# Performance work log

Measured on AMD Instinct MI355X. Metric: run time of the kernel, lower is better.

## Reference

```python
import jax, jax.numpy as jnp
import numpy as np

B, T, D = 4, 1024, 1024
H = 16
DH = D // H  # 64
NEG = jnp.float32(-2.0**32 + 1)


def _sinusoid_table(T, D):
    pos = np.arange(T)[:, None]
    i = np.arange(D)[None, :]
    angle = pos / np.power(10000.0, 2.0 * (i // 2) / D)
    tab = np.zeros((T, D))
    tab[:, 0::2] = np.sin(angle[:, 0::2])
    tab[:, 1::2] = np.cos(angle[:, 1::2])
    return jnp.asarray(tab, dtype=jnp.float32)


def setup_inputs() -> dict:
    key = jax.random.key(0)
    ks = jax.random.split(key, 10)
    inp = {
        "queries": jax.random.normal(ks[0], (B, T, D), dtype=jnp.float32),
        "keys": jax.random.normal(ks[1], (B, T, D), dtype=jnp.float32),
        "query_lens": jax.random.randint(ks[2], (B, 1), 1, T + 1),
        "key_lens": jax.random.randint(ks[3], (B, 1), 1, T + 1),
        # learned params
        "pe_q": _sinusoid_table(T, D),
        "pe_k": _sinusoid_table(T, D),
        "W_Query": jax.random.truncated_normal(ks[4], -2.0, 2.0, (D, D), dtype=jnp.float32) * 0.05,
        "W_key": jax.random.truncated_normal(ks[5], -2.0, 2.0, (D, D), dtype=jnp.float32) * 0.05,
        "W_Value": jax.random.truncated_normal(ks[6], -2.0, 2.0, (D, D), dtype=jnp.float32) * 0.05,
        "fw1": jax.random.normal(ks[7], (D, 4 * D), dtype=jnp.float32) * (1.0 / np.sqrt(D)),
        "fw2": jax.random.normal(ks[8], (4 * D, D), dtype=jnp.float32) * (1.0 / np.sqrt(4 * D)),
    }
    return inp


def _forward(queries, keys, pe_q, pe_k, W_Query, W_key, W_Value, fw1, fw2,
             query_lens, key_lens):
    scale = jnp.float32(np.sqrt(D))
    # positional encoding (scale=True). NOTE: source bug preserved —
    # keys tensor is overwritten by key_pe applied to the PE'd queries.
    q_in = queries + pe_q[None] * scale          # [B,T,D]
    k_in = q_in + pe_k[None] * scale             # [B,T,D]

    Q = q_in @ W_Query                           # [B,T,D]
    K = k_in @ W_key                             # [B,T,D]
    V = K @ W_Value                              # NOTE: V projected from projected keys (source quirk)

    def heads(x):  # [B,T,D] -> [H,B,T,DH]
        return x.reshape(B, T, H, DH).transpose(2, 0, 1, 3)

    Qh, Kh, Vh = heads(Q), heads(K), heads(V)
    scores = jnp.einsum("hbqd,hbkd->hbqk", Qh, Kh) / jnp.float32(np.sqrt(DH))

    t = jnp.arange(T)
    kmask = (t[None, :] < key_lens).astype(jnp.float32)    # [B,T]
    qmask = (t[None, :] < query_lens).astype(jnp.float32)  # [B,T]

    scores = jnp.where(kmask[None, :, None, :] == 1.0, scores, NEG)
    # blinding: set diagonal to large negative
    eye = jnp.eye(T, dtype=bool)
    scores = jnp.where(eye[None, None], NEG, scores)

    scores = scores - scores.max(axis=-1, keepdims=True)
    probs = jax.nn.softmax(scores, axis=-1)
    probs = probs * qmask[None, :, :, None]

    out = jnp.einsum("hbqk,hbkd->hbqd", probs, Vh)         # [H,B,T,DH]
    result = out.transpose(1, 2, 0, 3).reshape(B, T, D)
    result = result + q_in                                  # residual uses PE'd queries

    ff = jnp.maximum(result @ fw1, 0.0) @ fw2
    result = result + ff
    return result.mean(axis=1, keepdims=True)               # [B,1,D]


def reference(queries, keys, query_lens, key_lens, pe_q, pe_k,
              W_Query, W_key, W_Value, fw1, fw2):
    return _forward(queries, keys, pe_q, pe_k, W_Query, W_key, W_Value,
                    fw1, fw2, query_lens, key_lens)
```

## Files before the change

kernel.cpp:

```cpp
#include <hip/hip_runtime.h>

#define T_ 1024
#define D_ 1024
#define B_ 4
#define H_ 16
#define DH_ 64
#define M_ (B_*T_)
#define NEG_ (-4294967295.0f)

typedef __attribute__((ext_vector_type(8))) _Float16 f16x8;
typedef __attribute__((ext_vector_type(4))) float f32x4;

__device__ __forceinline__ unsigned short f2h(float f) {
    _Float16 h = (_Float16)f; unsigned short u; __builtin_memcpy(&u, &h, 2); return u;
}
__device__ __forceinline__ float h2f(unsigned short u) {
    _Float16 h; __builtin_memcpy(&h, &u, 2); return (float)h;
}

typedef const unsigned int __attribute__((address_space(1)))* gas_p;
typedef unsigned int __attribute__((address_space(3)))* las_p;
__device__ __forceinline__ void gl_lds16(const void* g, void* l) {
    __builtin_amdgcn_global_load_lds((gas_p)g, (las_p)l, 16, 0, 0);
}

__global__ __launch_bounds__(256) void conv_all(const float* __restrict__ q,
                                                const float* __restrict__ peq,
                                                const float* __restrict__ pek,
                                                const float* __restrict__ Wq,
                                                const float* __restrict__ Wk,
                                                const float* __restrict__ Wv,
                                                const float* __restrict__ fw1,
                                                const int* __restrict__ klv,
                                                unsigned short* __restrict__ A2,
                                                unsigned short* __restrict__ B2,
                                                unsigned short* __restrict__ WvT,
                                                unsigned short* __restrict__ fw1T)
{
    int blk = blockIdx.x;
    if (blk < 8192) {
        int i = blk * 256 + threadIdx.x;
        int m = i >> 8, c4 = (i & 255) << 2;
        int mq = m & 4095;
        if (m >= 4096) {
            int row = m - 4096;
            int kl = klv[row >> 10];
            if (kl > 1 && (row & 1023) >= kl) return;
        }
        float4 qv = *(const float4*)(q + (size_t)mq * D_ + c4);
        float4 p  = *(const float4*)(peq + (size_t)(m & (T_-1)) * D_ + c4);
        ushort4 h;
        if (m < 4096) {
            h.x = f2h(qv.x + 32.f*p.x); h.y = f2h(qv.y + 32.f*p.y);
            h.z = f2h(qv.z + 32.f*p.z); h.w = f2h(qv.w + 32.f*p.w);
        } else {
            float4 pk = *(const float4*)(pek + (size_t)(m & (T_-1)) * D_ + c4);
            h.x = f2h(qv.x + 32.f*(p.x + pk.x)); h.y = f2h(qv.y + 32.f*(p.y + pk.y));
            h.z = f2h(qv.z + 32.f*(p.z + pk.z)); h.w = f2h(qv.w + 32.f*(p.w + pk.w));
        }
        *(ushort4*)(A2 + (size_t)m * 1024 + c4) = h;
        return;
    }
    __shared__ float t[32][33];
    int r = threadIdx.x >> 5, c = threadIdx.x & 31;
    if (blk < 10240) {
        int l = blk - 8192;
        int z = l >> 10, k0 = ((l >> 5) & 31) * 32, n0 = (l & 31) * 32;
        const float* W = z ? Wk : Wq;
        #pragma unroll
        for (int rr = 0; rr < 4; ++rr)
            t[r + 8*rr][c] = W[(size_t)(k0 + r + 8*rr) * 1024 + n0 + c];
        __syncthreads();
        #pragma unroll
        for (int rr = 0; rr < 4; ++rr)
            B2[(size_t)(z * 1024 + n0 + r + 8*rr) * 1024 + k0 + c] = f2h(t[c][r + 8*rr]);
    } else if (blk < 11264) {
        int l = blk - 10240;
        int k0 = (l >> 5) * 32, n0 = (l & 31) * 32;
        #pragma unroll
        for (int rr = 0; rr < 4; ++rr)
            t[r + 8*rr][c] = Wv[(size_t)(k0 + r + 8*rr) * 1024 + n0 + c];
        __syncthreads();
        #pragma unroll
        for (int rr = 0; rr < 4; ++rr)
            WvT[(size_t)(n0 + r + 8*rr) * 1024 + k0 + c] = f2h(t[c][r + 8*rr]);
    } else {
        int l = blk - 11264;
        int k0 = (l >> 7) * 32, n0 = (l & 127) * 32;
        #pragma unroll
        for (int rr = 0; rr < 4; ++rr)
            t[r + 8*rr][c] = fw1[(size_t)(k0 + r + 8*rr) * 4096 + n0 + c];
        __syncthreads();
        #pragma unroll
        for (int rr = 0; rr < 4; ++rr)
            fw1T[(size_t)(n0 + r + 8*rr) * 1024 + k0 + c] = f2h(t[c][r + 8*rr]);
    }
}

template<int BM>
__global__ __launch_bounds__(256) void gemm_mfma(
    const unsigned short* __restrict__ A, int lda,
    const unsigned short* __restrict__ B, int ldb, int K,
    unsigned short* __restrict__ outh, unsigned short* __restrict__ outh2,
    int N, int flags,
    const int* __restrict__ qlv, const int* __restrict__ klv)
{
    constexpr int WN = (BM == 128) ? 2 : 4;
    constexpr int FN = 8 / WN;
    constexpr int NA = BM / 32;
    __shared__ __align__(16) unsigned short As[2][BM * 64];
    __shared__ __align__(16) unsigned short Bs[2][128 * 64];
    const int tid = threadIdx.x;
    const int m0 = blockIdx.y * BM, n0 = blockIdx.x << 7;
    if (flags & 32) {
        if (m0 < 4096) {
            if (n0 >= 1024) return;
            if ((m0 & 1023) >= qlv[m0 >> 10]) return;
        } else {
            if (n0 < 1024) return;
            int kl = klv[(m0 - 4096) >> 10];
            if (kl > 1 && (m0 & 1023) >= kl) return;
        }
    }
    if (flags & 256) {
        int bb = m0 >> 10, kl = klv[bb];
        if (kl > 1 && (m0 & 1023) >= kl) return;
    }
    const int lane = tid & 63, wave = tid >> 6;
    const int wm = (wave / WN) * 64;
    const int wn = (wave % WN) * (128 / WN);
    const int rl = lane & 15, kg = lane >> 4;
    const int rl7 = lane & 7;

    int ca[NA]; const unsigned short* gA[NA];
    #pragma unroll
    for (int i = 0; i < NA; ++i) {
        int c = i * 256 + tid;
        int row = c >> 3, k8 = (c & 7) ^ (row & 7);
        ca[i] = c * 8;
        gA[i] = A + (size_t)(m0 + row) * lda + k8 * 8;
    }
    int cb[4]; const unsigned short* gB[4];
    #pragma unroll
    for (int i = 0; i < 4; ++i) {
        int c = i * 256 + tid;
        int row = c >> 3, k8 = (c & 7) ^ (row & 7);
        cb[i] = c * 8;
        gB[i] = B + (size_t)(n0 + row) * ldb + k8 * 8;
    }

    int aoff[2][4], boff[2][FN];
    #pragma unroll
    for (int tt = 0; tt < 2; ++tt) {
        #pragma unroll
        for (int f = 0; f < 4; ++f)
            aoff[tt][f] = (wm + (f << 4) + rl) * 64 + (((tt * 4 + kg) ^ rl7) << 3);
        #pragma unroll
        for (int f = 0; f < FN; ++f)
            boff[tt][f] = (wn + (f << 4) + rl) * 64 + (((tt * 4 + kg) ^ rl7) << 3);
    }

    f32x4 acc[4][FN];
    #pragma unroll
    for (int i = 0; i < 4; ++i)
        #pragma unroll
        for (int j = 0; j < FN; ++j) {
            acc[i][j][0] = 0.f; acc[i][j][1] = 0.f;
            acc[i][j][2] = 0.f; acc[i][j][3] = 0.f;
        }

    const int NT = K >> 6;
    #pragma unroll
    for (int i = 0; i < 4; ++i)  gl_lds16(gB[i], &Bs[0][cb[i]]);
    #pragma unroll
    for (int i = 0; i < NA; ++i) gl_lds16(gA[i], &As[0][ca[i]]);
    #pragma unroll
    for (int i = 0; i < 4; ++i)  gl_lds16(gB[i] + 64, &Bs[1][cb[i]]);
    #pragma unroll
    for (int i = 0; i < NA; ++i) gl_lds16(gA[i] + 64, &As[1][ca[i]]);

    for (int t = 0; t < NT; ++t) {
        const int cur = t & 1;
        if (t + 1 < NT) {
            if constexpr (BM == 128) asm volatile("s_waitcnt vmcnt(8)" ::: "memory");
            else                     asm volatile("s_waitcnt vmcnt(6)" ::: "memory");
        } else {
            asm volatile("s_waitcnt vmcnt(0)" ::: "memory");
        }
        __builtin_amdgcn_s_barrier();
        __builtin_amdgcn_sched_barrier(0);
        f16x8 av[2][4], bv[2][FN];
        #pragma unroll
        for (int tt = 0; tt < 2; ++tt) {
            #pragma unroll
            for (int f = 0; f < 4; ++f)
                av[tt][f] = *(const f16x8*)&As[cur][aoff[tt][f]];
            #pragma unroll
            for (int f = 0; f < FN; ++f)
                bv[tt][f] = *(const f16x8*)&Bs[cur][boff[tt][f]];
        }
        asm volatile("s_waitcnt lgkmcnt(0)" ::: "memory");
        __builtin_amdgcn_sched_barrier(0);
        __builtin_amdgcn_s_barrier();
        __builtin_amdgcn_sched_barrier(0);
        if (t + 2 < NT) {
            const int ko = (t + 2) << 6;
            #pragma unroll
            for (int i = 0; i < 4; ++i)  gl_lds16(gB[i] + ko, &Bs[cur][cb[i]]);
            #pragma unroll
            for (int i = 0; i < NA; ++i) gl_lds16(gA[i] + ko, &As[cur][ca[i]]);
        }
        #pragma unroll
        for (int fm = 0; fm < 4; ++fm)
            #pragma unroll
            for (int fn = 0; fn < FN; ++fn) {
                acc[fm][fn] = __builtin_amdgcn_mfma_f32_16x16x32_f16(av[0][fm], bv[0][fn], acc[fm][fn], 0, 0, 0);
                acc[fm][fn] = __builtin_amdgcn_mfma_f32_16x16x32_f16(av[1][fm], bv[1][fn], acc[fm][fn], 0, 0, 0);
            }
    }

    #pragma unroll
    for (int fm = 0; fm < 4; ++fm) {
        int row = m0 + wm + (fm << 4) + (kg << 2);
        #pragma unroll
        for (int fn = 0; fn < FN; ++fn) {
            int col = n0 + wn + (fn << 4) + rl;
            if (flags & 64) {
                ushort4 u;
                u.x = f2h(acc[fm][fn][0]); u.y = f2h(acc[fm][fn][1]);
                u.z = f2h(acc[fm][fn][2]); u.w = f2h(acc[fm][fn][3]);
                size_t a = ((size_t)((row >> 10) * 16 + (col >> 6)) * 64 + (col & 63)) * 1024 + (row & 1023);
                *(ushort4*)(outh + a) = u;
                continue;
            }
            #pragma unroll
            for (int r = 0; r < 4; ++r) {
                float x = acc[fm][fn][r];
                int rr = row + r;
                if (flags & 32) {
                    if (rr < 4096) outh[(size_t)rr * 1024 + col] = f2h(x);
                    else           outh2[(size_t)(rr - 4096) * 1024 + (col - 1024)] = f2h(x);
                } else if (flags & 16) {
                    outh[(size_t)rr * N + col] = f2h(x);
                }
            }
        }
    }
}

__global__ __launch_bounds__(512, 2) void ffn1_8p(
    const unsigned short* __restrict__ A,
    const unsigned short* __restrict__ B,
    float* __restrict__ hpart)
{
    __shared__ __align__(16) unsigned short As[2][16384];
    __shared__ __align__(16) unsigned short Bs[2][16384];
    __shared__ float hp[8][64];
    const int tid = threadIdx.x;
    const int m0 = blockIdx.y << 8, n0 = blockIdx.x << 8;
    const int lane = tid & 63, wave = tid >> 6;
    const int wm = wave >> 2, wn = wave & 3;
    const int rl = lane & 15, kg = lane >> 4, rl7 = lane & 7;

    const int row0 = tid >> 3;
    const int k8c = (tid & 7) ^ (row0 & 7);
    const int cs0 = tid * 8;
    const int gofs = row0 * 1024 + k8c * 8;
    const unsigned short* Ap = A + (size_t)m0 * 1024 + gofs;
    const unsigned short* Bp = B + (size_t)n0 * 1024 + gofs;

    const int base_a = ((wm * 128 + rl) * 8 + (kg ^ rl7)) * 8;
    const int base_b = (((wn >> 1) * 128 + (wn & 1) * 64 + rl) * 8 + (kg ^ rl7)) * 8;

    f32x4 acc[8][4];
    #pragma unroll
    for (int i = 0; i < 8; ++i)
        #pragma unroll
        for (int j = 0; j < 4; ++j) {
            acc[i][j][0] = 0.f; acc[i][j][1] = 0.f;
            acc[i][j][2] = 0.f; acc[i][j][3] = 0.f;
        }

    const int NT = 16;
    #pragma unroll
    for (int i = 0; i < 4; ++i) gl_lds16(Ap + i * 65536, &As[0][cs0 + i * 4096]);
    #pragma unroll
    for (int i = 0; i < 4; ++i) gl_lds16(Bp + i * 65536, &Bs[0][cs0 + i * 4096]);
    #pragma unroll
    for (int i = 0; i < 4; ++i) gl_lds16(Ap + i * 65536 + 64, &As[1][cs0 + i * 4096]);
    #pragma unroll
    for (int i = 0; i < 4; ++i) gl_lds16(Bp + i * 65536 + 64, &Bs[1][cs0 + i * 4096]);

    for (int t = 0; t < NT; ++t) {
        const int cur = t & 1;
        if (t + 1 < NT) asm volatile("s_waitcnt vmcnt(8)" ::: "memory");
        else            asm volatile("s_waitcnt vmcnt(0)" ::: "memory");
        __builtin_amdgcn_s_barrier();
        __builtin_amdgcn_sched_barrier(0);
        f16x8 av[8][2], bv[4][2];
        #pragma unroll
        for (int f = 0; f < 8; ++f) {
            int o = base_a + f * 1024;
            av[f][0] = *(const f16x8*)&As[cur][o];
            av[f][1] = *(const f16x8*)&As[cur][o ^ 32];
        }
        #pragma unroll
        for (int fn = 0; fn < 4; ++fn) {
            int o = base_b + fn * 1024;
            bv[fn][0] = *(const f16x8*)&Bs[cur][o];
            bv[fn][1] = *(const f16x8*)&Bs[cur][o ^ 32];
        }
        asm volatile("s_waitcnt lgkmcnt(0)" ::: "memory");
        __builtin_amdgcn_sched_barrier(0);
        __builtin_amdgcn_s_barrier();
        __builtin_amdgcn_sched_barrier(0);
        const bool pre = (t + 2 < NT);
        const int ko = (t + 2) << 6;
        #pragma unroll
        for (int p = 0; p < 4; ++p) {
            if (pre) {
                if (p < 2) {
                    gl_lds16(Ap + (2*p) * 65536 + ko,     &As[cur][cs0 + (2*p) * 4096]);
                    gl_lds16(Ap + (2*p + 1) * 65536 + ko, &As[cur][cs0 + (2*p + 1) * 4096]);
                } else {
                    gl_lds16(Bp + (2*p - 4) * 65536 + ko, &Bs[cur][cs0 + (2*p - 4) * 4096]);
                    gl_lds16(Bp + (2*p - 3) * 65536 + ko, &Bs[cur][cs0 + (2*p - 3) * 4096]);
                }
            }
            __builtin_amdgcn_sched_barrier(0);
            __builtin_amdgcn_s_setprio(1);
            #pragma unroll
            for (int f = 2 * p; f < 2 * p + 2; ++f)
                #pragma unroll
                for (int fn = 0; fn < 4; ++fn) {
                    acc[f][fn] = __builtin_amdgcn_mfma_f32_16x16x32_f16(av[f][0], bv[fn][0], acc[f][fn], 0, 0, 0);
                    acc[f][fn] = __builtin_amdgcn_mfma_f32_16x16x32_f16(av[f][1], bv[fn][1], acc[f][fn], 0, 0, 0);
                }
            __builtin_amdgcn_s_setprio(0);
            __builtin_amdgcn_sched_barrier(0);
        }
    }

    #pragma unroll
    for (int fn = 0; fn < 4; ++fn) {
        float p = 0.f;
        #pragma unroll
        for (int f = 0; f < 8; ++f)
            #pragma unroll
            for (int r = 0; r < 4; ++r) p += fmaxf(acc[f][fn][r], 0.f);
        p += __shfl_xor(p, 16);
        p += __shfl_xor(p, 32);
        if (kg == 0) hp[wave][fn * 16 + rl] = p;
    }
    __syncthreads();
    if (tid < 256) {
        int wn2 = tid >> 6, cc = tid & 63;
        float s = hp[wn2][cc] + hp[wn2 + 4][cc];
        hpart[(size_t)blockIdx.y * 4096 + n0 + wn2 * 64 + cc] = s;
    }
}

__global__ __launch_bounds__(256) void attn_mfma(
    const unsigned short* __restrict__ Qh,
    const unsigned short* __restrict__ Kh,
    const unsigned short* __restrict__ Vt,
    unsigned short* __restrict__ q16,
    const int* __restrict__ qlens, const int* __restrict__ klens)
{
    __shared__ __align__(16) unsigned short KS[2][4096];
    __shared__ __align__(16) unsigned short VtS[2][4096];
    __shared__ __align__(16) unsigned short Pl[4][1152];

    const int tid = threadIdx.x;
    const int bh = blockIdx.x & 63;
    const int qt = blockIdx.x >> 6;
    const int b = bh >> 4, h = bh & 15;
    const int qbase = qt * 64;
    const int qlen = qlens[b], klen = klens[b];
    if (qbase >= qlen) return;

    const int lane = tid & 63, wq = tid >> 6;
    const int rl = lane & 15, kg = lane >> 4, rl7 = lane & 7;
    const int gq = qbase + wq * 16 + rl;

    f16x8 qb[2];
    {
        const unsigned short* p1 = Qh + (size_t)(b * 1024 + gq) * 1024 + h * 64 + kg * 8;
        qb[0] = *(const f16x8*)p1;  qb[1] = *(const f16x8*)(p1 + 32);
    }

    const unsigned short* gK[2]; const unsigned short* gV[2];
    int cs[2];
    #pragma unroll
    for (int i = 0; i < 2; ++i) {
        int c = i * 256 + tid;
        int row = c >> 3, ch = (c & 7) ^ (row & 7);
        cs[i] = c * 8;
        gK[i] = Kh + (size_t)(b * 1024 + row) * 1024 + h * 64 + ch * 8;
        gV[i] = Vt + (size_t)(bh * 64 + row) * 1024 + ch * 8;
    }

    int akoff[4][2];
    #pragma unroll
    for (int mf = 0; mf < 4; ++mf)
        #pragma unroll
        for (int kh = 0; kh < 2; ++kh)
            akoff[mf][kh] = (mf * 16 + rl) * 64 + (((kg + 4 * kh) ^ rl7) << 3);

    f32x4 o[4];
    #pragma unroll
    for (int i = 0; i < 4; ++i) { o[i][0]=0.f; o[i][1]=0.f; o[i][2]=0.f; o[i][3]=0.f; }
    float m_run = -3.0e38f, l_run = 0.f;
    const int nt = (klen == 1) ? (T_ / 64) : ((klen + 63) >> 6);

    gl_lds16(gK[0], &KS[0][cs[0]]);
    gl_lds16(gK[1], &KS[0][cs[1]]);
    gl_lds16(gV[0], &VtS[0][cs[0]]);
    gl_lds16(gV[1], &VtS[0][cs[1]]);
    gl_lds16(gK[0] + 65536, &KS[1][cs[0]]);
    gl_lds16(gK[1] + 65536, &KS[1][cs[1]]);
    gl_lds16(gV[0] + 64,    &VtS[1][cs[0]]);
    gl_lds16(gV[1] + 64,    &VtS[1][cs[1]]);

    for (int kb = 0; kb < nt; ++kb) {
        const int cur = kb & 1;
        const int kbase = kb * 64;
        if (kb + 1 < nt) asm volatile("s_waitcnt vmcnt(4)" ::: "memory");
        else             asm volatile("s_waitcnt vmcnt(0)" ::: "memory");
        __builtin_amdgcn_s_barrier();
        __builtin_amdgcn_sched_barrier(0);

        float v[4][4];
        __builtin_amdgcn_s_setprio(1);
        #pragma unroll
        for (int mf = 0; mf < 4; ++mf) {
            f32x4 s; s[0]=0.f; s[1]=0.f; s[2]=0.f; s[3]=0.f;
            f16x8 a0 = *(const f16x8*)&KS[cur][akoff[mf][0]];
            f16x8 a1 = *(const f16x8*)&KS[cur][akoff[mf][1]];
            s = __builtin_amdgcn_mfma_f32_16x16x32_f16(a0, qb[0], s, 0, 0, 0);
            s = __builtin_amdgcn_mfma_f32_16x16x32_f16(a1, qb[1], s, 0, 0, 0);
            #pragma unroll
            for (int r = 0; r < 4; ++r) {
                int gk = kbase + mf * 16 + kg * 4 + r;
                float x = s[r] * 0.125f;
                if (gk >= klen || gk == gq) x = NEG_;
                v[mf][r] = x;
            }
        }
        __builtin_amdgcn_s_setprio(0);
        float mt = -3.0e38f;
        #pragma unroll
        for (int mf = 0; mf < 4; ++mf)
            #pragma unroll
            for (int r = 0; r < 4; ++r) mt = fmaxf(mt, v[mf][r]);
        mt = fmaxf(mt, __shfl_xor(mt, 16));
        mt = fmaxf(mt, __shfl_xor(mt, 32));
        float mnew = fmaxf(m_run, mt);
        float fac = __expf(m_run - mnew);
        float sum = 0.f;
        #pragma unroll
        for (int mf = 0; mf < 4; ++mf) {
            ushort4 pb;
            pb.x = f2h(__expf(v[mf][0] - mnew));
            pb.y = f2h(__expf(v[mf][1] - mnew));
            pb.z = f2h(__expf(v[mf][2] - mnew));
            pb.w = f2h(__expf(v[mf][3] - mnew));
            sum += h2f(pb.x) + h2f(pb.y) + h2f(pb.z) + h2f(pb.w);
            *(ushort4*)&Pl[wq][rl * 72 + mf * 16 + kg * 4] = pb;
        }
        sum += __shfl_xor(sum, 16);
        sum += __shfl_xor(sum, 32);
        l_run = l_run * fac + sum;
        m_run = mnew;
        #pragma unroll
        for (int i = 0; i < 4; ++i) {
            o[i][0] *= fac; o[i][1] *= fac; o[i][2] *= fac; o[i][3] *= fac;
        }
        f16x8 bp0 = *(const f16x8*)&Pl[wq][rl * 72 + kg * 8];
        f16x8 bp1 = *(const f16x8*)&Pl[wq][rl * 72 + 32 + kg * 8];
        __builtin_amdgcn_s_setprio(1);
        #pragma unroll
        for (int dmf = 0; dmf < 4; ++dmf) {
            f16x8 a0 = *(const f16x8*)&VtS[cur][akoff[dmf][0]];
            f16x8 a1 = *(const f16x8*)&VtS[cur][akoff[dmf][1]];
            o[dmf] = __builtin_amdgcn_mfma_f32_16x16x32_f16(a0, bp0, o[dmf], 0, 0, 0);
            o[dmf] = __builtin_amdgcn_mfma_f32_16x16x32_f16(a1, bp1, o[dmf], 0, 0, 0);
        }
        __builtin_amdgcn_s_setprio(0);
        __builtin_amdgcn_s_barrier();
        __builtin_amdgcn_sched_barrier(0);
        if (kb + 2 < nt) {
            const size_t ko = (size_t)(kbase + 128) * 1024;
            gl_lds16(gK[0] + ko, &KS[cur][cs[0]]);
            gl_lds16(gK[1] + ko, &KS[cur][cs[1]]);
            gl_lds16(gV[0] + kbase + 128, &VtS[cur][cs[0]]);
            gl_lds16(gV[1] + kbase + 128, &VtS[cur][cs[1]]);
        }
    }

    float invl = (gq < qlen) ? (1.f / l_run) : 0.f;
    #pragma unroll
    for (int dmf = 0; dmf < 4; ++dmf)
        #pragma unroll
        for (int r = 0; r < 4; ++r) {
            int dh = dmf * 16 + kg * 4 + r;
            size_t a = (size_t)(b * 1024 + gq) * 1024 + h * 64 + dh;
            q16[a] = f2h(o[dmf][r] * invl + h2f(q16[a]));
        }
}

__global__ __launch_bounds__(256) void mean16(const unsigned short* __restrict__ X,
                                              float* __restrict__ out, int Xdim)
{
    __shared__ float red[4][128];
    int tid = threadIdx.x;
    int b = blockIdx.y;
    int dbase = blockIdx.x * 128;
    int tq = tid >> 6, dd = tid & 63;
    int d = dbase + dd * 2;
    const unsigned short* p = X + ((size_t)b * T_ + tq * 256) * Xdim + d;
    float s0 = 0.f, s1 = 0.f;
    for (int t = 0; t < 256; ++t) {
        ushort2 v = *(const ushort2*)(p + (size_t)t * Xdim);
        s0 += h2f(v.x); s1 += h2f(v.y);
    }
    red[tq][dd*2] = s0; red[tq][dd*2 + 1] = s1;
    __syncthreads();
    if (tq == 0) {
        float a = red[0][dd*2] + red[1][dd*2] + red[2][dd*2] + red[3][dd*2];
        float c = red[0][dd*2+1] + red[1][dd*2+1] + red[2][dd*2+1] + red[3][dd*2+1];
        out[(size_t)b * Xdim + d]     = a * (1.f/1024.f);
        out[(size_t)b * Xdim + d + 1] = c * (1.f/1024.f);
    }
}

__global__ __launch_bounds__(256) void final_partial(const float* __restrict__ Hpart,
                                                     const float* __restrict__ fw2,
                                                     float* __restrict__ Pout)
{
    __shared__ float red[4][4][64];
    __shared__ float hm[4][128];
    int tid = threadIdx.x;
    #pragma unroll
    for (int s = 0; s < 2; ++s) {
        int idx = s * 256 + tid;
        int bb = idx >> 7, jl = idx & 127;
        int j = blockIdx.y * 128 + jl;
        float acc = 0.f;
        #pragma unroll
        for (int i = 0; i < 4; ++i)
            acc += Hpart[((size_t)(bb * 4 + i)) * 4096 + j];
        hm[bb][jl] = acc * (1.f / 1024.f);
    }
    __syncthreads();
    int dd = tid & 63;
    int d = blockIdx.x * 64 + dd;
    int jq = tid >> 6;
    float s4[4] = {0.f, 0.f, 0.f, 0.f};
    for (int jj = 0; jj < 32; ++jj) {
        int jl = jq * 32 + jj;
        int j = blockIdx.y * 128 + jl;
        float wv = fw2[(size_t)j * 1024 + d];
        s4[0] += hm[0][jl] * wv;
        s4[1] += hm[1][jl] * wv;
        s4[2] += hm[2][jl] * wv;
        s4[3] += hm[3][jl] * wv;
    }
    #pragma unroll
    for (int bb = 0; bb < 4; ++bb) red[jq][bb][dd] = s4[bb];
    __syncthreads();
    if (jq == 0) {
        #pragma unroll
        for (int bb = 0; bb < 4; ++bb) {
            float tot = red[0][bb][dd] + red[1][bb][dd] + red[2][bb][dd] + red[3][bb][dd];
            Pout[((size_t)blockIdx.y * 4 + bb) * 1024 + d] = tot;
        }
    }
}

__global__ __launch_bounds__(256) void reduce_out(const float* __restrict__ Mres,
                                                  const float* __restrict__ Pout,
                                                  float* __restrict__ out)
{
    int idx = blockIdx.x * 256 + threadIdx.x;
    int b = idx >> 10, d = idx & 1023;
    float s = Mres[(size_t)b * 1024 + d];
    #pragma unroll
    for (int jy = 0; jy < 32; ++jy)
        s += Pout[((size_t)jy * 4 + b) * 1024 + d];
    out[(size_t)b * 1024 + d] = s;
}

extern "C" void kernel_launch(void* const* d_in, const int* in_sizes, int n_in,
                              void* d_out, int out_size, void* d_ws, size_t ws_size,
                              hipStream_t stream)
{
    const float* queries = (const float*)d_in[0];
    const int*   qlens   = (const int*)d_in[2];
    const int*   klens   = (const int*)d_in[3];
    const float* pe_q    = (const float*)d_in[4];
    const float* pe_k    = (const float*)d_in[5];
    const float* Wq      = (const float*)d_in[6];
    const float* Wk      = (const float*)d_in[7];
    const float* Wv      = (const float*)d_in[8];
    const float* fw1     = (const float*)d_in[9];
    const float* fw2     = (const float*)d_in[10];
    float* out = (float*)d_out;

    char* w = (char*)d_ws;
    unsigned short* Qh   = (unsigned short*)(w);
    unsigned short* A2   = (unsigned short*)(w + (8ll  << 20));
    unsigned short* q16  = A2;
    unsigned short* Kh16 = (unsigned short*)(w + (24ll << 20));
    unsigned short* B2   = (unsigned short*)(w + (32ll << 20));
    unsigned short* WvT  = (unsigned short*)(w + (36ll << 20));
    unsigned short* Vt   = (unsigned short*)(w + (38ll << 20));
    unsigned short* fw1T = (unsigned short*)(w + (46ll << 20));
    float*          Hpart= (float*)(w + (54ll << 20));
    float*          Mres = (float*)(w + (55ll << 20));
    float*          Pout = (float*)(w + (56ll << 20));

    conv_all<<<15360, 256, 0, stream>>>(queries, pe_q, pe_k, Wq, Wk, Wv, fw1, klens,
                                        A2, B2, WvT, fw1T);
    gemm_mfma<128><<<dim3(16, 64), 256, 0, stream>>>(
        A2, 1024, B2, 1024, 1024,
        Qh, Kh16, 2048, 32, qlens, klens);
    gemm_mfma<64><<<dim3(8, 64), 256, 0, stream>>>(
        Kh16, 1024, WvT, 1024, 1024,
        Vt, nullptr, 1024, 64 | 256, nullptr, klens);
    attn_mfma<<<1024, 256, 0, stream>>>(Qh, Kh16, Vt, q16, qlens, klens);
    ffn1_8p<<<dim3(16, 16), 512, 0, stream>>>(q16, fw1T, Hpart);
    mean16<<<dim3(8, 4), 256, 0, stream>>>(q16, Mres, 1024);
    final_partial<<<dim3(16, 32), 256, 0, stream>>>(Hpart, fw2, Pout);
    reduce_out<<<16, 256, 0, stream>>>(Mres, Pout, out);
}
```

Baseline: 125.3 us.

## Use 256x256 8-wave tiles for QK projection and fuse mean into tail kernel

Replaces the generic 128x128 GEMM for the fused Q/K projection with a dedicated 512-thread kernel that computes 256x256 tiles, interleaves prefetch with MFMA groups and raises wave priority around them. This is meant to raise data reuse per LDS load and overlap memory with compute. The V projection becomes its own specialised kernel. The mean kernel is merged into the final_partial kernel as an extra grid row, saving one launch. Larger tiles coarsen the early-exit granularity for masked rows and reduce the number of blocks.

```diff
diff --git a/kernel.cpp b/kernel.cpp
--- a/kernel.cpp
+++ b/kernel.cpp
@@ -97,38 +97,142 @@
     }
 }
 
-template<int BM>
-__global__ __launch_bounds__(256) void gemm_mfma(
-    const unsigned short* __restrict__ A, int lda,
-    const unsigned short* __restrict__ B, int ldb, int K,
-    unsigned short* __restrict__ outh, unsigned short* __restrict__ outh2,
-    int N, int flags,
+__global__ __launch_bounds__(512, 2) void qk_8p(
+    const unsigned short* __restrict__ A,
+    const unsigned short* __restrict__ B,
+    unsigned short* __restrict__ Qh, unsigned short* __restrict__ Kh16,
     const int* __restrict__ qlv, const int* __restrict__ klv)
 {
-    constexpr int WN = (BM == 128) ? 2 : 4;
-    constexpr int FN = 8 / WN;
-    constexpr int NA = BM / 32;
+    __shared__ __align__(16) unsigned short As[2][16384];
+    __shared__ __align__(16) unsigned short Bs[2][16384];
+    const int tid = threadIdx.x;
+    const int m0 = blockIdx.y << 8, n0 = blockIdx.x << 8;
+    if (m0 < 4096) {
+        if (n0 >= 1024) return;
+        if ((m0 & 1023) >= qlv[m0 >> 10]) return;
+    } else {
+        if (n0 < 1024) return;
+        int kl = klv[(m0 - 4096) >> 10];
+        if (kl > 1 && (m0 & 1023) >= kl) return;
+    }
+    const int lane = tid & 63, wave = tid >> 6;
+    const int wm = wave >> 2, wn = wave & 3;
+    const int rl = lane & 15, kg = lane >> 4, rl7 = lane & 7;
+
+    const int row0 = tid >> 3;
+    const int k8c = (tid & 7) ^ (row0 & 7);
+    const int cs0 = tid * 8;
+    const int gofs = row0 * 1024 + k8c * 8;
+    const unsigned short* Ap = A + (size_t)m0 * 1024 + gofs;
+    const unsigned short* Bp = B + (size_t)n0 * 1024 + gofs;
+
+    const int base_a = ((wm * 128 + rl) * 8 + (kg ^ rl7)) * 8;
+    const int base_b = (((wn >> 1) * 128 + (wn & 1) * 64 + rl) * 8 + (kg ^ rl7)) * 8;
+
+    f32x4 acc[8][4];
+    #pragma unroll
+    for (int i = 0; i < 8; ++i)
+        #pragma unroll
+        for (int j = 0; j < 4; ++j) {
+            acc[i][j][0] = 0.f; acc[i][j][1] = 0.f;
+            acc[i][j][2] = 0.f; acc[i][j][3] = 0.f;
+        }
+
+    const int NT = 16;
+    #pragma unroll
+    for (int i = 0; i < 4; ++i) gl_lds16(Ap + i * 65536, &As[0][cs0 + i * 4096]);
+    #pragma unroll
+    for (int i = 0; i < 4; ++i) gl_lds16(Bp + i * 65536, &Bs[0][cs0 + i * 4096]);
+    #pragma unroll
+    for (int i = 0; i < 4; ++i) gl_lds16(Ap + i * 65536 + 64, &As[1][cs0 + i * 4096]);
+    #pragma unroll
+    for (int i = 0; i < 4; ++i) gl_lds16(Bp + i * 65536 + 64, &Bs[1][cs0 + i * 4096]);
+
+    for (int t = 0; t < NT; ++t) {
+        const int cur = t & 1;
+        if (t + 1 < NT) asm volatile("s_waitcnt vmcnt(8)" ::: "memory");
+        else            asm volatile("s_waitcnt vmcnt(0)" ::: "memory");
+        __builtin_amdgcn_s_barrier();
+        __builtin_amdgcn_sched_barrier(0);
+        f16x8 av[8][2], bv[4][2];
+        #pragma unroll
+        for (int f = 0; f < 8; ++f) {
+            int o = base_a + f * 1024;
+            av[f][0] = *(const f16x8*)&As[cur][o];
+            av[f][1] = *(const f16x8*)&As[cur][o ^ 32];
+        }
+        #pragma unroll
+        for (int fn = 0; fn < 4; ++fn) {
+            int o = base_b + fn * 1024;
+            bv[fn][0] = *(const f16x8*)&Bs[cur][o];
+            bv[fn][1] = *(const f16x8*)&Bs[cur][o ^ 32];
+        }
+        asm volatile("s_waitcnt lgkmcnt(0)" ::: "memory");
+        __builtin_amdgcn_sched_barrier(0);
+        __builtin_amdgcn_s_barrier();
+        __builtin_amdgcn_sched_barrier(0);
+        const bool pre = (t + 2 < NT);
+        const int ko = (t + 2) << 6;
+        #pragma unroll
+        for (int p = 0; p < 4; ++p) {
+            if (pre) {
+                if (p < 2) {
+                    gl_lds16(Ap + (2*p) * 65536 + ko,     &As[cur][cs0 + (2*p) * 4096]);
+                    gl_lds16(Ap + (2*p + 1) * 65536 + ko, &As[cur][cs0 + (2*p + 1) * 4096]);
+                } else {
+                    gl_lds16(Bp + (2*p - 4) * 65536 + ko, &Bs[cur][cs0 + (2*p - 4) * 4096]);
+                    gl_lds16(Bp + (2*p - 3) * 65536 + ko, &Bs[cur][cs0 + (2*p - 3) * 4096]);
+                }
+            }
+            __builtin_amdgcn_sched_barrier(0);
+            __builtin_amdgcn_s_setprio(1);
+            #pragma unroll
+            for (int f = 2 * p; f < 2 * p + 2; ++f)
+                #pragma unroll
+                for (int fn = 0; fn < 4; ++fn) {
+                    acc[f][fn] = __builtin_amdgcn_mfma_f32_16x16x32_f16(av[f][0], bv[fn][0], acc[f][fn], 0, 0, 0);
+                    acc[f][fn] = __builtin_amdgcn_mfma_f32_16x16x32_f16(av[f][1], bv[fn][1], acc[f][fn], 0, 0, 0);
+                }
+            __builtin_amdgcn_s_setprio(0);
+            __builtin_amdgcn_sched_barrier(0);
+        }
+    }
+
+    const bool isQ = (m0 < 4096);
+    #pragma unroll
+    for (int f = 0; f < 8; ++f) {
+        int row = m0 + wm * 128 + f * 16 + (kg << 2);
+        #pragma unroll
+        for (int fn = 0; fn < 4; ++fn) {
+            int col = n0 + wn * 64 + fn * 16 + rl;
+            #pragma unroll
+            for (int r = 0; r < 4; ++r) {
+                unsigned short val = f2h(acc[f][fn][r]);
+                if (isQ) Qh[(size_t)(row + r) * 1024 + col] = val;
+                else     Kh16[(size_t)(row + r - 4096) * 1024 + (col - 1024)] = val;
+            }
+        }
+    }
+}
+
+__global__ __launch_bounds__(256) void gemm_v(
+    const unsigned short* __restrict__ A,
+    const unsigned short* __restrict__ B,
+    unsigned short* __restrict__ Vt,
+    const int* __restrict__ klv)
+{
+    constexpr int BM = 64, WN = 4, FN = 2, NA = 2;
     __shared__ __align__(16) unsigned short As[2][BM * 64];
     __shared__ __align__(16) unsigned short Bs[2][128 * 64];
     const int tid = threadIdx.x;
     const int m0 = blockIdx.y * BM, n0 = blockIdx.x << 7;
-    if (flags & 32) {
-        if (m0 < 4096) {
-            if (n0 >= 1024) return;
-            if ((m0 & 1023) >= qlv[m0 >> 10]) return;
-        } else {
-            if (n0 < 1024) return;
-            int kl = klv[(m0 - 4096) >> 10];
-            if (kl > 1 && (m0 & 1023) >= kl) return;
-        }
-    }
-    if (flags & 256) {
+    {
         int bb = m0 >> 10, kl = klv[bb];
         if (kl > 1 && (m0 & 1023) >= kl) return;
     }
     const int lane = tid & 63, wave = tid >> 6;
-    const int wm = (wave / WN) * 64;
-    const int wn = (wave % WN) * (128 / WN);
+    const int wm = 0;
+    const int wn = wave * 32;
     const int rl = lane & 15, kg = lane >> 4;
     const int rl7 = lane & 7;
 
@@ -138,7 +242,7 @@
         int c = i * 256 + tid;
         int row = c >> 3, k8 = (c & 7) ^ (row & 7);
         ca[i] = c * 8;
-        gA[i] = A + (size_t)(m0 + row) * lda + k8 * 8;
+        gA[i] = A + (size_t)(m0 + row) * 1024 + k8 * 8;
     }
     int cb[4]; const unsigned short* gB[4];
     #pragma unroll
@@ -146,7 +250,7 @@
         int c = i * 256 + tid;
         int row = c >> 3, k8 = (c & 7) ^ (row & 7);
         cb[i] = c * 8;
-        gB[i] = B + (size_t)(n0 + row) * ldb + k8 * 8;
+        gB[i] = B + (size_t)(n0 + row) * 1024 + k8 * 8;
     }
 
     int aoff[2][4], boff[2][FN];
@@ -169,7 +273,7 @@
             acc[i][j][2] = 0.f; acc[i][j][3] = 0.f;
         }
 
-    const int NT = K >> 6;
+    const int NT = 16;
     #pragma unroll
     for (int i = 0; i < 4; ++i)  gl_lds16(gB[i], &Bs[0][cb[i]]);
     #pragma unroll
@@ -181,12 +285,8 @@
 
     for (int t = 0; t < NT; ++t) {
         const int cur = t & 1;
-        if (t + 1 < NT) {
-            if constexpr (BM == 128) asm volatile("s_waitcnt vmcnt(8)" ::: "memory");
-            else                     asm volatile("s_waitcnt vmcnt(6)" ::: "memory");
-        } else {
-            asm volatile("s_waitcnt vmcnt(0)" ::: "memory");
-        }
+        if (t + 1 < NT) asm volatile("s_waitcnt vmcnt(6)" ::: "memory");
+        else            asm volatile("s_waitcnt vmcnt(0)" ::: "memory");
         __builtin_amdgcn_s_barrier();
         __builtin_amdgcn_sched_barrier(0);
         f16x8 av[2][4], bv[2][FN];
@@ -225,27 +325,162 @@
         #pragma unroll
         for (int fn = 0; fn < FN; ++fn) {
             int col = n0 + wn + (fn << 4) + rl;
-            if (flags & 64) {
-                ushort4 u;
-                u.x = f2h(acc[fm][fn][0]); u.y = f2h(acc[fm][fn][1]);
-                u.z = f2h(acc[fm][fn][2]); u.w = f2h(acc[fm][fn][3]);
-                size_t a = ((size_t)((row >> 10) * 16 + (col >> 6)) * 64 + (col & 63)) * 1024 + (row & 1023);
-                *(ushort4*)(outh + a) = u;
-                continue;
+            ushort4 u;
+            u.x = f2h(acc[fm][fn][0]); u.y = f2h(acc[fm][fn][1]);
+            u.z = f2h(acc[fm][fn][2]); u.w = f2h(acc[fm][fn][3]);
+            size_t a = ((size_t)((row >> 10) * 16 + (col >> 6)) * 64 + (col & 63)) * 1024 + (row & 1023);
+            *(ushort4*)(Vt + a) = u;
+        }
+    }
+}
+
+__global__ __launch_bounds__(256) void attn_mfma(
+    const unsigned short* __restrict__ Qh,
+    const unsigned short* __restrict__ Kh,
+    const unsigned short* __restrict__ Vt,
+    unsigned short* __restrict__ q16,
+    const int* __restrict__ qlens, const int* __restrict__ klens)
+{
+    __shared__ __align__(16) unsigned short KS[2][4096];
+    __shared__ __align__(16) unsigned short VtS[2][4096];
+    __shared__ __align__(16) unsigned short Pl[4][1152];
+
+    const int tid = threadIdx.x;
+    const int bh = blockIdx.x & 63;
+    const int qt = blockIdx.x >> 6;
+    const int b = bh >> 4, h = bh & 15;
+    const int qbase = qt * 64;
+    const int qlen = qlens[b], klen = klens[b];
+    if (qbase >= qlen) return;
+
+    const int lane = tid & 63, wq = tid >> 6;
+    const int rl = lane & 15, kg = lane >> 4, rl7 = lane & 7;
+    const int gq = qbase + wq * 16 + rl;
+
+    f16x8 qb[2];
+    {
+        const unsigned short* p1 = Qh + (size_t)(b * 1024 + gq) * 1024 + h * 64 + kg * 8;
+        qb[0] = *(const f16x8*)p1;  qb[1] = *(const f16x8*)(p1 + 32);
+    }
+
+    const unsigned short* gK[2]; const unsigned short* gV[2];
+    int cs[2];
+    #pragma unroll
+    for (int i = 0; i < 2; ++i) {
+        int c = i * 256 + tid;
+        int row = c >> 3, ch = (c & 7) ^ (row & 7);
+        cs[i] = c * 8;
+        gK[i] = Kh + (size_t)(b * 1024 + row) * 1024 + h * 64 + ch * 8;
+        gV[i] = Vt + (size_t)(bh * 64 + row) * 1024 + ch * 8;
+    }
+
+    int akoff[4][2];
+    #pragma unroll
+    for (int mf = 0; mf < 4; ++mf)
+        #pragma unroll
+        for (int kh = 0; kh < 2; ++kh)
+            akoff[mf][kh] = (mf * 16 + rl) * 64 + (((kg + 4 * kh) ^ rl7) << 3);
+
+    f32x4 o[4];
+    #pragma unroll
+    for (int i = 0; i < 4; ++i) { o[i][0]=0.f; o[i][1]=0.f; o[i][2]=0.f; o[i][3]=0.f; }
+    float m_run = -3.0e38f, l_run = 0.f;
+    const int nt = (klen == 1) ? (T_ / 64) : ((klen + 63) >> 6);
+
+    gl_lds16(gK[0], &KS[0][cs[0]]);
+    gl_lds16(gK[1], &KS[0][cs[1]]);
+    gl_lds16(gV[0], &VtS[0][cs[0]]);
+    gl_lds16(gV[1], &VtS[0][cs[1]]);
+    gl_lds16(gK[0] + 65536, &KS[1][cs[0]]);
+    gl_lds16(gK[1] + 65536, &KS[1][cs[1]]);
+    gl_lds16(gV[0] + 64,    &VtS[1][cs[0]]);
+    gl_lds16(gV[1] + 64,    &VtS[1][cs[1]]);
+
+    for (int kb = 0; kb < nt; ++kb) {
+        const int cur = kb & 1;
+        const int kbase = kb * 64;
+        if (kb + 1 < nt) asm volatile("s_waitcnt vmcnt(4)" ::: "memory");
+        else             asm volatile("s_waitcnt vmcnt(0)" ::: "memory");
+        __builtin_amdgcn_s_barrier();
+        __builtin_amdgcn_sched_barrier(0);
+
+        float v[4][4];
+        __builtin_amdgcn_s_setprio(1);
+        #pragma unroll
+        for (int mf = 0; mf < 4; ++mf) {
+            f32x4 s; s[0]=0.f; s[1]=0.f; s[2]=0.f; s[3]=0.f;
+            f16x8 a0 = *(const f16x8*)&KS[cur][akoff[mf][0]];
+            f16x8 a1 = *(const f16x8*)&KS[cur][akoff[mf][1]];
+            s = __builtin_amdgcn_mfma_f32_16x16x32_f16(a0, qb[0], s, 0, 0, 0);
+            s = __builtin_amdgcn_mfma_f32_16x16x32_f16(a1, qb[1], s, 0, 0, 0);
+            #pragma unroll
+            for (int r = 0; r < 4; ++r) {
+                int gk = kbase + mf * 16 + kg * 4 + r;
+                float x = s[r] * 0.125f;
+                if (gk >= klen || gk == gq) x = NEG_;
+                v[mf][r] = x;
             }
-            #pragma unroll
-            for (int r = 0; r < 4; ++r) {
-                float x = acc[fm][fn][r];
-                int rr = row + r;
-                if (flags & 32) {
-                    if (rr < 4096) outh[(size_t)rr * 1024 + col] = f2h(x);
-                    else           outh2[(size_t)(rr - 4096) * 1024 + (col - 1024)] = f2h(x);
-                } else if (flags & 16) {
-                    outh[(size_t)rr * N + col] = f2h(x);
-                }
-            }
-        }
-    }
+        }
+        __builtin_amdgcn_s_setprio(0);
+        float mt = -3.0e38f;
+        #pragma unroll
+        for (int mf = 0; mf < 4; ++mf)
+            #pragma unroll
+            for (int r = 0; r < 4; ++r) mt = fmaxf(mt, v[mf][r]);
+        mt = fmaxf(mt, __shfl_xor(mt, 16));
+        mt = fmaxf(mt, __shfl_xor(mt, 32));
+        float mnew = fmaxf(m_run, mt);
+        float fac = __expf(m_run - mnew);
+        float sum = 0.f;
+        #pragma unroll
+        for (int mf = 0; mf < 4; ++mf) {
+            ushort4 pb;
+            pb.x = f2h(__expf(v[mf][0] - mnew));
+            pb.y = f2h(__expf(v[mf][1] - mnew));
+            pb.z = f2h(__expf(v[mf][2] - mnew));
+            pb.w = f2h(__expf(v[mf][3] - mnew));
+            sum += h2f(pb.x) + h2f(pb.y) + h2f(pb.z) + h2f(pb.w);
+            *(ushort4*)&Pl[wq][rl * 72 + mf * 16 + kg * 4] = pb;
+        }
+        sum += __shfl_xor(sum, 16);
+        sum += __shfl_xor(sum, 32);
+        l_run = l_run * fac + sum;
+        m_run = mnew;
+        #pragma unroll
+        for (int i = 0; i < 4; ++i) {
+            o[i][0] *= fac; o[i][1] *= fac; o[i][2] *= fac; o[i][3] *= fac;
+        }
+        f16x8 bp0 = *(const f16x8*)&Pl[wq][rl * 72 + kg * 8];
+        f16x8 bp1 = *(const f16x8*)&Pl[wq][rl * 72 + 32 + kg * 8];
+        __builtin_amdgcn_s_setprio(1);
+        #pragma unroll
+        for (int dmf = 0; dmf < 4; ++dmf) {
+            f16x8 a0 = *(const f16x8*)&VtS[cur][akoff[dmf][0]];
+            f16x8 a1 = *(const f16x8*)&VtS[cur][akoff[dmf][1]];
+            o[dmf] = __builtin_amdgcn_mfma_f32_16x16x32_f16(a0, bp0, o[dmf], 0, 0, 0);
+            o[dmf] = __builtin_amdgcn_mfma_f32_16x16x32_f16(a1, bp1, o[dmf], 0, 0, 0);
+        }
+        __builtin_amdgcn_s_setprio(0);
+        __builtin_amdgcn_s_barrier();
+        __builtin_amdgcn_sched_barrier(0);
+        if (kb + 2 < nt) {
+            const size_t ko = (size_t)(kbase + 128) * 1024;
+            gl_lds16(gK[0] + ko, &KS[cur][cs[0]]);
+            gl_lds16(gK[1] + ko, &KS[cur][cs[1]]);
+            gl_lds16(gV[0] + kbase + 128, &VtS[cur][cs[0]]);
+            gl_lds16(gV[1] + kbase + 128, &VtS[cur][cs[1]]);
+        }
+    }
+
+    float invl = (gq < qlen) ? (1.f / l_run) : 0.f;
+    #pragma unroll
+    for (int dmf = 0; dmf < 4; ++dmf)
+        #pragma unroll
+        for (int r = 0; r < 4; ++r) {
+            int dh = dmf * 16 + kg * 4 + r;
+            size_t a = (size_t)(b * 1024 + gq) * 1024 + h * 64 + dh;
+            q16[a] = f2h(o[dmf][r] * invl + h2f(q16[a]));
+        }
 }
 
 __global__ __launch_bounds__(512, 2) void ffn1_8p(
@@ -360,187 +595,38 @@
     }
 }
 
-__global__ __launch_bounds__(256) void attn_mfma(
-    const unsigned short* __restrict__ Qh,
-    const unsigned short* __restrict__ Kh,
-    const unsigned short* __restrict__ Vt,
-    unsigned short* __restrict__ q16,
-    const int* __restrict__ qlens, const int* __restrict__ klens)
+__global__ __launch_bounds__(256) void tail(const unsigned short* __restrict__ q16,
+                                            const float* __restrict__ Hpart,
+                                            const float* __restrict__ fw2,
+                                            float* __restrict__ Pout,
+                                            float* __restrict__ Mres)
 {
-    __shared__ __align__(16) unsigned short KS[2][4096];
-    __shared__ __align__(16) unsigned short VtS[2][4096];
-    __shared__ __align__(16) unsigned short Pl[4][1152];
-
-    const int tid = threadIdx.x;
-    const int bh = blockIdx.x & 63;
-    const int qt = blockIdx.x >> 6;
-    const int b = bh >> 4, h = bh & 15;
-    const int qbase = qt * 64;
-    const int qlen = qlens[b], klen = klens[b];
-    if (qbase >= qlen) return;
-
-    const int lane = tid & 63, wq = tid >> 6;
-    const int rl = lane & 15, kg = lane >> 4, rl7 = lane & 7;
-    const int gq = qbase + wq * 16 + rl;
-
-    f16x8 qb[2];
-    {
-        const unsigned short* p1 = Qh + (size_t)(b * 1024 + gq) * 1024 + h * 64 + kg * 8;
-        qb[0] = *(const f16x8*)p1;  qb[1] = *(const f16x8*)(p1 + 32);
-    }
-
-    const unsigned short* gK[2]; const unsigned short* gV[2];
-    int cs[2];
-    #pragma unroll
-    for (int i = 0; i < 2; ++i) {
-        int c = i * 256 + tid;
-        int row = c >> 3, ch = (c & 7) ^ (row & 7);
-        cs[i] = c * 8;
-        gK[i] = Kh + (size_t)(b * 1024 + row) * 1024 + h * 64 + ch * 8;
-        gV[i] = Vt + (size_t)(bh * 64 + row) * 1024 + ch * 8;
-    }
-
-    int akoff[4][2];
-    #pragma unroll
-    for (int mf = 0; mf < 4; ++mf)
-        #pragma unroll
-        for (int kh = 0; kh < 2; ++kh)
-            akoff[mf][kh] = (mf * 16 + rl) * 64 + (((kg + 4 * kh) ^ rl7) << 3);
-
-    f32x4 o[4];
-    #pragma unroll
-    for (int i = 0; i < 4; ++i) { o[i][0]=0.f; o[i][1]=0.f; o[i][2]=0.f; o[i][3]=0.f; }
-    float m_run = -3.0e38f, l_run = 0.f;
-    const int nt = (klen == 1) ? (T_ / 64) : ((klen + 63) >> 6);
-
-    gl_lds16(gK[0], &KS[0][cs[0]]);
-    gl_lds16(gK[1], &KS[0][cs[1]]);
-    gl_lds16(gV[0], &VtS[0][cs[0]]);
-    gl_lds16(gV[1], &VtS[0][cs[1]]);
-    gl_lds16(gK[0] + 65536, &KS[1][cs[0]]);
-    gl_lds16(gK[1] + 65536, &KS[1][cs[1]]);
-    gl_lds16(gV[0] + 64,    &VtS[1][cs[0]]);
-    gl_lds16(gV[1] + 64,    &VtS[1][cs[1]]);
-
-    for (int kb = 0; kb < nt; ++kb) {
-        const int cur = kb & 1;
-        const int kbase = kb * 64;
-        if (kb + 1 < nt) asm volatile("s_waitcnt vmcnt(4)" ::: "memory");
-        else             asm volatile("s_waitcnt vmcnt(0)" ::: "memory");
-        __builtin_amdgcn_s_barrier();
-        __builtin_amdgcn_sched_barrier(0);
-
-        float v[4][4];
-        __builtin_amdgcn_s_setprio(1);
-        #pragma unroll
-        for (int mf = 0; mf < 4; ++mf) {
-            f32x4 s; s[0]=0.f; s[1]=0.f; s[2]=0.f; s[3]=0.f;
-            f16x8 a0 = *(const f16x8*)&KS[cur][akoff[mf][0]];
-            f16x8 a1 = *(const f16x8*)&KS[cur][akoff[mf][1]];
-            s = __builtin_amdgcn_mfma_f32_16x16x32_f16(a0, qb[0], s, 0, 0, 0);
-            s = __builtin_amdgcn_mfma_f32_16x16x32_f16(a1, qb[1], s, 0, 0, 0);
-            #pragma unroll
-            for (int r = 0; r < 4; ++r) {
-                int gk = kbase + mf * 16 + kg * 4 + r;
-                float x = s[r] * 0.125f;
-                if (gk >= klen || gk == gq) x = NEG_;
-                v[mf][r] = x;
+    int tid = threadIdx.x;
+    if (blockIdx.y == 32) {
+        __shared__ float red[4][256];
+        int b = blockIdx.x >> 2;
+        int dbase = (blockIdx.x & 3) * 256;
+        int tq = tid >> 6, dd = tid & 63;
+        int d = dbase + dd * 4;
+        const unsigned short* p = q16 + ((size_t)b * T_ + tq * 256) * 1024 + d;
+        float s0 = 0.f, s1 = 0.f, s2 = 0.f, s3 = 0.f;
+        for (int t = 0; t < 256; ++t) {
+            ushort4 v = *(const ushort4*)(p + (size_t)t * 1024);
+            s0 += h2f(v.x); s1 += h2f(v.y); s2 += h2f(v.z); s3 += h2f(v.w);
+        }
+        red[tq][dd*4] = s0; red[tq][dd*4+1] = s1; red[tq][dd*4+2] = s2; red[tq][dd*4+3] = s3;
+        __syncthreads();
+        if (tq == 0) {
+            #pragma unroll
+            for (int j = 0; j < 4; ++j) {
+                float a = red[0][dd*4+j] + red[1][dd*4+j] + red[2][dd*4+j] + red[3][dd*4+j];
+                Mres[(size_t)b * 1024 + d + j] = a * (1.f/1024.f);
             }
         }
-        __builtin_amdgcn_s_setprio(0);
-        float mt = -3.0e38f;
-        #pragma unroll
-        for (int mf = 0; mf < 4; ++mf)
-            #pragma unroll
-            for (int r = 0; r < 4; ++r) mt = fmaxf(mt, v[mf][r]);
-        mt = fmaxf(mt, __shfl_xor(mt, 16));
-        mt = fmaxf(mt, __shfl_xor(mt, 32));
-        float mnew = fmaxf(m_run, mt);
-        float fac = __expf(m_run - mnew);
-        float sum = 0.f;
-        #pragma unroll
-        for (int mf = 0; mf < 4; ++mf) {
-            ushort4 pb;
-            pb.x = f2h(__expf(v[mf][0] - mnew));
-            pb.y = f2h(__expf(v[mf][1] - mnew));
-            pb.z = f2h(__expf(v[mf][2] - mnew));
-            pb.w = f2h(__expf(v[mf][3] - mnew));
-            sum += h2f(pb.x) + h2f(pb.y) + h2f(pb.z) + h2f(pb.w);
-            *(ushort4*)&Pl[wq][rl * 72 + mf * 16 + kg * 4] = pb;
-        }
-        sum += __shfl_xor(sum, 16);
-        sum += __shfl_xor(sum, 32);
-        l_run = l_run * fac + sum;
-        m_run = mnew;
-        #pragma unroll
-        for (int i = 0; i < 4; ++i) {
-            o[i][0] *= fac; o[i][1] *= fac; o[i][2] *= fac; o[i][3] *= fac;
-        }
-        f16x8 bp0 = *(const f16x8*)&Pl[wq][rl * 72 + kg * 8];
-        f16x8 bp1 = *(const f16x8*)&Pl[wq][rl * 72 + 32 + kg * 8];
-        __builtin_amdgcn_s_setprio(1);
-        #pragma unroll
-        for (int dmf = 0; dmf < 4; ++dmf) {
-            f16x8 a0 = *(const f16x8*)&VtS[cur][akoff[dmf][0]];
-            f16x8 a1 = *(const f16x8*)&VtS[cur][akoff[dmf][1]];
-            o[dmf] = __builtin_amdgcn_mfma_f32_16x16x32_f16(a0, bp0, o[dmf], 0, 0, 0);
-            o[dmf] = __builtin_amdgcn_mfma_f32_16x16x32_f16(a1, bp1, o[dmf], 0, 0, 0);
-        }
-        __builtin_amdgcn_s_setprio(0);
-        __builtin_amdgcn_s_barrier();
-        __builtin_amdgcn_sched_barrier(0);
-        if (kb + 2 < nt) {
-            const size_t ko = (size_t)(kbase + 128) * 1024;
-            gl_lds16(gK[0] + ko, &KS[cur][cs[0]]);
-            gl_lds16(gK[1] + ko, &KS[cur][cs[1]]);
-            gl_lds16(gV[0] + kbase + 128, &VtS[cur][cs[0]]);
-            gl_lds16(gV[1] + kbase + 128, &VtS[cur][cs[1]]);
-        }
-    }
-
-    float invl = (gq < qlen) ? (1.f / l_run) : 0.f;
-    #pragma unroll
-    for (int dmf = 0; dmf < 4; ++dmf)
-        #pragma unroll
-        for (int r = 0; r < 4; ++r) {
-            int dh = dmf * 16 + kg * 4 + r;
-            size_t a = (size_t)(b * 1024 + gq) * 1024 + h * 64 + dh;
-            q16[a] = f2h(o[dmf][r] * invl + h2f(q16[a]));
-        }
-}
-
-__global__ __launch_bounds__(256) void mean16(const unsigned short* __restrict__ X,
-                                              float* __restrict__ out, int Xdim)
-{
-    __shared__ float red[4][128];
-    int tid = threadIdx.x;
-    int b = blockIdx.y;
-    int dbase = blockIdx.x * 128;
-    int tq = tid >> 6, dd = tid & 63;
-    int d = dbase + dd * 2;
-    const unsigned short* p = X + ((size_t)b * T_ + tq * 256) * Xdim + d;
-    float s0 = 0.f, s1 = 0.f;
-    for (int t = 0; t < 256; ++t) {
-        ushort2 v = *(const ushort2*)(p + (size_t)t * Xdim);
-        s0 += h2f(v.x); s1 += h2f(v.y);
-    }
-    red[tq][dd*2] = s0; red[tq][dd*2 + 1] = s1;
-    __syncthreads();
-    if (tq == 0) {
-        float a = red[0][dd*2] + red[1][dd*2] + red[2][dd*2] + red[3][dd*2];
-        float c = red[0][dd*2+1] + red[1][dd*2+1] + red[2][dd*2+1] + red[3][dd*2+1];
-        out[(size_t)b * Xdim + d]     = a * (1.f/1024.f);
-        out[(size_t)b * Xdim + d + 1] = c * (1.f/1024.f);
-    }
-}
-
-__global__ __launch_bounds__(256) void final_partial(const float* __restrict__ Hpart,
-                                                     const float* __restrict__ fw2,
-                                                     float* __restrict__ Pout)
-{
+        return;
+    }
     __shared__ float red[4][4][64];
     __shared__ float hm[4][128];
-    int tid = threadIdx.x;
     #pragma unroll
     for (int s = 0; s < 2; ++s) {
         int idx = s * 256 + tid;
@@ -622,15 +708,10 @@
 
     conv_all<<<15360, 256, 0, stream>>>(queries, pe_q, pe_k, Wq, Wk, Wv, fw1, klens,
                                         A2, B2, WvT, fw1T);
-    gemm_mfma<128><<<dim3(16, 64), 256, 0, stream>>>(
-        A2, 1024, B2, 1024, 1024,
-        Qh, Kh16, 2048, 32, qlens, klens);
-    gemm_mfma<64><<<dim3(8, 64), 256, 0, stream>>>(
-        Kh16, 1024, WvT, 1024, 1024,
-        Vt, nullptr, 1024, 64 | 256, nullptr, klens);
+    qk_8p<<<dim3(8, 32), 512, 0, stream>>>(A2, B2, Qh, Kh16, qlens, klens);
+    gemm_v<<<dim3(8, 64), 256, 0, stream>>>(Kh16, WvT, Vt, klens);
     attn_mfma<<<1024, 256, 0, stream>>>(Qh, Kh16, Vt, q16, qlens, klens);
     ffn1_8p<<<dim3(16, 16), 512, 0, stream>>>(q16, fw1T, Hpart);
-    mean16<<<dim3(8, 4), 256, 0, stream>>>(q16, Mres, 1024);
-    final_partial<<<dim3(16, 32), 256, 0, stream>>>(Hpart, fw2, Pout);
+    tail<<<dim3(16, 33), 256, 0, stream>>>(q16, Hpart, fw2, Pout, Mres);
     reduce_out<<<16, 256, 0, stream>>>(Mres, Pout, out);
 }
```

New measurement: 128.0 us. +2.2%, slower.
